# Performance work log

Measured on AMD Instinct MI355X. Metric: run time of the kernel, lower is better.

The kernel has to match this reference:

```python
import jax, jax.numpy as jnp
import numpy as np

THRESH = 0.5
POOL_K = 8  # feature_hw // proto_grid = 128 // 16
EPS = 1e-4
NEG = -1e30


def _avg_pool(x, k):
    # x: [n, c, h, w] -> [n, c, h//k, w//k]
    n, c, h, w = x.shape
    return x.reshape(n, c, h // k, k, w // k, k).mean(axis=(3, 5))


def reference(qry, sup_x, sup_y):
    # squeeze as in forward
    qry = qry[:, 0]          # [B=1, C, H, W]
    sup_x = sup_x[0, :, 0]   # [shot, C, H, W]
    sup_y = sup_y[0]         # [shot, 1, H, W]

    shot, nch, H, W = sup_x.shape

    # grid prototypes via avg pooling
    n_sup = _avg_pool(sup_x, POOL_K)                      # [shot, C, gh, gw]
    y_g = _avg_pool(sup_y, POOL_K)                        # [shot, 1, gh, gw]

    cand = n_sup.reshape(shot, nch, -1).transpose(0, 2, 1).reshape(-1, nch)  # [M, C]
    y_flat = y_g.reshape(-1)                              # [M]

    # threshold mask with fallback chain (thresh -> 0.1 -> all), static shapes
    m1 = y_flat > THRESH
    m2 = y_flat > 0.1
    m_all = jnp.ones_like(m1)
    mask = jnp.where(jnp.any(m1), m1, jnp.where(jnp.any(m2), m2, m_all))  # [M]

    # mean-center and safe L2-normalize prototypes (per proto over channels)
    protos = cand - cand.mean(axis=-1, keepdims=True)
    pro_n = protos / jnp.maximum(jnp.linalg.norm(protos, axis=1, keepdims=True), EPS)  # [M, C]

    # mean-center and safe L2-normalize query (per pixel over channels)
    qc = qry - qry.mean(axis=1, keepdims=True)
    qry_n = qc / jnp.maximum(jnp.linalg.norm(qc, axis=1, keepdims=True), EPS)          # [B, C, H, W]

    # cosine-sim 1x1 conv = GEMM, scaled
    dists = jnp.einsum('bchw,mc->bmhw', qry_n, pro_n) * 20.0                           # [B, M, H, W]

    # masked softmax over prototypes (equivalent to selecting masked subset)
    logits = jnp.where(mask[None, :, None, None], dists, NEG)
    prob = jax.nn.softmax(logits, axis=1)                                              # [B, M, H, W]

    # weighted back-projection and final similarity map
    ch_proto = jnp.einsum('mc,bmhw->bchw', pro_n, prob)                                # [B, C, H, W]
    pred_grid = jnp.sum(qry_n * ch_proto * 20.0, axis=1, keepdims=True)                # [B, 1, H, W]
    return pred_grid


def setup_inputs() -> dict:
    key = jax.random.key(0)
    k1, k2, k3 = jax.random.split(key, 3)
    qry = jax.random.normal(k1, (1, 1, 256, 128, 128), dtype=jnp.float32)
    sup_x = jax.random.normal(k2, (1, 5, 1, 256, 128, 128), dtype=jnp.float32)
    sup_y = jax.random.uniform(k3, (1, 5, 1, 128, 128), dtype=jnp.float32)
    return {"qry": qry, "sup_x": sup_x, "sup_y": sup_y}
```

## Files before the change

kernel.cpp:

```cpp
#include <hip/hip_runtime.h>
#include <math.h>

typedef _Float16 f16x8 __attribute__((ext_vector_type(8)));
typedef float f32x4 __attribute__((ext_vector_type(4)));


__global__ __launch_bounds__(256) void pool_kernel(const float* __restrict__ sup_x,
                                                   const float* __restrict__ sup_y,
                                                   _Float16* __restrict__ pro_raw,
                                                   float* __restrict__ psum,
                                                   float* __restrict__ yv_ws) {
    const int b = blockIdx.x, t = threadIdx.x;
    if (b < 640) {
        __shared__ float hs[8192];
        __shared__ float xa[16][33];
        const int s = b >> 7, rem = b & 127;
        const int gy = rem >> 3, cq = rem & 7;
        const float* base = sup_x + ((size_t)(s * 256 + cq * 32) * 128 + gy * 8) * 128;
#pragma unroll 8
        for (int i = 0; i < 32; ++i) {
            const int run = i * 8 + (t >> 5);
            const float4 v = *(const float4*)(base + ((size_t)(run >> 3) * 128 + (run & 7)) * 128 + (t & 31) * 4);
            hs[i * 256 + t] = v.x + v.y + v.z + v.w;
        }
        __syncthreads();
#pragma unroll
        for (int e0 = 0; e0 < 2; ++e0) {
            const int e = e0 * 256 + t;
            const int c = e >> 4, gx = e & 15;
            float sum = 0.f;
#pragma unroll
            for (int r = 0; r < 8; ++r)
                sum += hs[(c * 8 + r) * 32 + gx * 2] + hs[(c * 8 + r) * 32 + gx * 2 + 1];
            xa[gx][c] = sum * (1.f / 64.f);
        }
        __syncthreads();
        const int mbase = s * 256 + gy * 16;
        if (t < 64) {
            const int gx = t >> 2, gi = t & 3;
            const int m = mbase + gx;
            const int g = cq * 4 + gi;
            f16x8 hv;
#pragma unroll
            for (int j = 0; j < 8; ++j) hv[j] = (_Float16)xa[gx][gi * 8 + j];
            *(f16x8*)(pro_raw + (size_t)m * 256 + ((g ^ (m & 7)) << 3)) = hv;
        } else if (t < 80) {
            const int gx = t - 64;
            float s1 = 0.f, s2 = 0.f;
#pragma unroll
            for (int c = 0; c < 32; ++c) { const float x = xa[gx][c]; s1 += x; s2 += x * x; }
            const int m = mbase + gx;
            psum[m * 16 + cq * 2]     = s1;
            psum[m * 16 + cq * 2 + 1] = s2;
        }
    } else {
        const int r = b - 640;
        const int gy = t >> 4, gx = t & 15;
        const float* base = sup_y + r * 16384 + gy * 1024 + gx * 8;
        float sum = 0.f;
#pragma unroll
        for (int rr = 0; rr < 8; ++rr) {
            const float4 a = *(const float4*)(base + rr * 128);
            const float4 bb = *(const float4*)(base + rr * 128 + 4);
            sum += a.x + a.y + a.z + a.w + bb.x + bb.y + bb.z + bb.w;
        }
        yv_ws[r * 256 + t] = sum * (1.f / 64.f);
    }
}

__device__ __forceinline__ void gload_lds16h(const _Float16* g, _Float16* l) {
    __builtin_amdgcn_global_load_lds((const __attribute__((address_space(1))) unsigned int*)g,
                                     (__attribute__((address_space(3))) unsigned int*)l,
                                     16, 0, 0);
}
__device__ __forceinline__ void gload_lds16f(const float* g, float* l) {
    __builtin_amdgcn_global_load_lds((const __attribute__((address_space(1))) unsigned int*)g,
                                     (__attribute__((address_space(3))) unsigned int*)l,
                                     16, 0, 0);
}

__device__ __forceinline__ void stage_tile(const _Float16* __restrict__ pro_raw,
                                           int tile, _Float16* dst, int w, int l) {
#pragma unroll
    for (int i = 0; i < 8; ++i) {
        const int off = w * 4096 + i * 512 + l * 8;
        gload_lds16h(pro_raw + (size_t)tile * 32768 + off, dst + off);
    }
}

__device__ __forceinline__ void compute_tile(const _Float16* __restrict__ pb,
                                             const float* __restrict__ msp,
                                             const float* __restrict__ asp,
                                             const f16x8 (&bfr)[4][8],
                                             int row, int ln7, int lq,
                                             float (&Sa)[4], float (&Wa)[4]) {
    f32x4 acc[4];
#pragma unroll
    for (int p = 0; p < 4; ++p) acc[p] = (f32x4){0.f, 0.f, 0.f, 0.f};
#pragma unroll
    for (int ks = 0; ks < 8; ++ks) {
        const int ch = (ks * 4 + lq) ^ ln7;
        const f16x8 a = *(const f16x8*)(pb + row * 256 + ch * 8);
#pragma unroll
        for (int p = 0; p < 4; ++p)
            acc[p] = __builtin_amdgcn_mfma_f32_16x16x32_f16(a, bfr[p][ks], acc[p], 0, 0, 0);
    }
    const f32x4 mkv = *(const f32x4*)(msp + lq * 4);
    const f32x4 av  = *(const f32x4*)(asp + lq * 4);
#pragma unroll
    for (int p = 0; p < 4; ++p) {
        float ssum = 0.f, wsum = 0.f;
#pragma unroll
        for (int r = 0; r < 4; ++r) {
            const float d = av[r] * acc[p][r];
            const float e = mkv[r] * __expf(d - 20.f);
            ssum += e; wsum += e * d;
        }
        Sa[p] += ssum; Wa[p] += wsum;
    }
}

__global__ __launch_bounds__(512, 2) void main_kernel(const float* __restrict__ qry,
                                                      const _Float16* __restrict__ pro_raw,
                                                      const float* __restrict__ psum,
                                                      const float* __restrict__ yv_ws,
                                                      float* __restrict__ out) {
    __shared__ __align__(16) _Float16 arena[65536];
    __shared__ float ms[1280];
    __shared__ float alf[1280];
    __shared__ float scr[1024];
    __shared__ float2 stats[64];
    __shared__ int iflags[2];

    float*     qtf  = (float*)arena;
    _Float16*  qs   = arena + 32768;
    _Float16*  buf0 = arena;
    _Float16*  buf1 = arena + 32768;
    float*     red  = (float*)arena;

    const int t = threadIdx.x;
    const int w = t >> 6, l = t & 63;
    const int ln = l & 15, lq = l >> 4;
    const int ln7 = ln & 7;
    const int px0 = blockIdx.x * 64;

    if (t < 2) iflags[t] = 0;
    __syncthreads();

#pragma unroll
    for (int i = 0; i < 8; ++i) {
        const int c = i * 32 + (t >> 4);
        gload_lds16f(qry + (size_t)c * 16384 + px0 + (t & 15) * 4,
                     qtf + i * 2048 + t * 4);
    }

    float yv3[3];
    int f0 = 0, f1 = 0;
#pragma unroll
    for (int k = 0; k < 3; ++k) {
        const int m = t + k * 512;
        if (m < 1280) {
            const f32x4 p0 = *(const f32x4*)(psum + m * 16);
            const f32x4 p1 = *(const f32x4*)(psum + m * 16 + 4);
            const f32x4 p2 = *(const f32x4*)(psum + m * 16 + 8);
            const f32x4 p3 = *(const f32x4*)(psum + m * 16 + 12);
            const float S1 = p0[0] + p0[2] + p1[0] + p1[2] + p2[0] + p2[2] + p3[0] + p3[2];
            const float S2 = p0[1] + p0[3] + p1[1] + p1[3] + p2[1] + p2[3] + p3[1] + p3[3];
            alf[m] = 20.f / fmaxf(sqrtf(fmaxf(S2 - S1 * S1 * (1.f / 256.f), 0.f)), 1e-4f);
            const float y = yv_ws[m];
            yv3[k] = y;
            if (y > 0.5f) f0 = 1;
            if (y > 0.1f) f1 = 1;
        }
    }
    if (f0) atomicOr(&iflags[0], 1);
    if (f1) atomicOr(&iflags[1], 1);
    __syncthreads();
    {
        const int mode = iflags[0] ? 0 : (iflags[1] ? 1 : 2);
#pragma unroll
        for (int k = 0; k < 3; ++k) {
            const int m = t + k * 512;
            if (m < 1280)
                ms[m] = (mode == 0) ? (yv3[k] > 0.5f ? 1.f : 0.f)
                      : (mode == 1) ? (yv3[k] > 0.1f ? 1.f : 0.f) : 1.f;
        }
    }

    {
        const int p = t & 63, q = t >> 6;
        float s1 = 0.f, s2 = 0.f;
        for (int cc = 0; cc < 32; ++cc) {
            const float x = qtf[(q * 32 + cc) * 64 + p];
            s1 += x; s2 += x * x;
        }
        scr[q * 64 + p] = s1; scr[512 + q * 64 + p] = s2;
    }
    __syncthreads();
    if (t < 64) {
        float S1 = 0.f, S2 = 0.f;
        for (int q = 0; q < 8; ++q) { S1 += scr[q * 64 + t]; S2 += scr[512 + q * 64 + t]; }
        const float mu = S1 * (1.f / 256.f);
        const float nrm = sqrtf(fmaxf(S2 - 256.f * mu * mu, 0.f));
        stats[t] = make_float2(mu, 1.f / fmaxf(nrm, 1e-4f));
    }
    __syncthreads();
    {
        const int px = t & 63, e = t >> 6;
        const float2 st = stats[px];
#pragma unroll
        for (int u = 0; u < 4; ++u) {
            const int g = e * 4 + u;
            f16x8 hv;
#pragma unroll
            for (int j = 0; j < 8; ++j)
                hv[j] = (_Float16)((qtf[(g * 8 + j) * 64 + px] - st.x) * st.y);
            *(f16x8*)(qs + px * 256 + ((g ^ (px & 7)) << 3)) = hv;
        }
    }
    __syncthreads();

    stage_tile(pro_raw, 0, buf0, w, l);

    f16x8 bfr[4][8];
#pragma unroll
    for (int p = 0; p < 4; ++p) {
        const int px = p * 16 + ln;
        const int sB = px & 7;
#pragma unroll
        for (int ks = 0; ks < 8; ++ks) {
            const int g = ks * 4 + lq;
            bfr[p][ks] = *(const f16x8*)(qs + px * 256 + ((g ^ sB) << 3));
        }
    }
    __syncthreads();

    stage_tile(pro_raw, 1, buf1, w, l);

    const int row = w * 16 + ln;
    float Sa[4] = {0.f, 0.f, 0.f, 0.f}, Wa[4] = {0.f, 0.f, 0.f, 0.f};

#pragma unroll 1
    for (int tile = 0; tile < 10; ++tile) {
        if (tile < 8) asm volatile("s_waitcnt vmcnt(8)" ::: "memory");
        else          asm volatile("s_waitcnt vmcnt(0)" ::: "memory");
        compute_tile((tile & 1) ? buf1 : buf0,
                     ms + tile * 128 + w * 16, alf + tile * 128 + w * 16,
                     bfr, row, ln7, lq, Sa, Wa);
        if (tile < 8) {
            asm volatile("s_waitcnt lgkmcnt(0)" ::: "memory");
            __builtin_amdgcn_sched_barrier(0);
            stage_tile(pro_raw, tile + 2, (tile & 1) ? buf1 : buf0, w, l);
        }
    }

    __syncthreads();
#pragma unroll
    for (int p = 0; p < 4; ++p) {
        const int px = p * 16 + ln;
        const int slot = (w * 4 + lq + px) & 31;
        red[px * 32 + slot] = Sa[p];
        red[2048 + px * 32 + slot] = Wa[p];
    }
    __syncthreads();
    if (t < 64) {
        float S = 0.f, W = 0.f;
        for (int s = 0; s < 32; ++s) {
            const int slot = (s + t) & 31;
            S += red[t * 32 + slot];
            W += red[2048 + t * 32 + slot];
        }
        out[px0 + t] = W / S;
    }
}

extern "C" void kernel_launch(void* const* d_in, const int* in_sizes, int n_in,
                              void* d_out, int out_size, void* d_ws, size_t ws_size,
                              hipStream_t stream) {
    const float* qry   = (const float*)d_in[0];
    const float* sup_x = (const float*)d_in[1];
    const float* sup_y = (const float*)d_in[2];
    float* out = (float*)d_out;

    char* ws = (char*)d_ws;
    _Float16*  pro_raw = (_Float16*)ws;           ws += 1280 * 256 * 2;
    float*     psum    = (float*)ws;              ws += 1280 * 16 * 4;
    float*     yv_ws   = (float*)ws;

    pool_kernel<<<645, 256, 0, stream>>>(sup_x, sup_y, pro_raw, psum, yv_ws);
    main_kernel<<<256, 512, 0, stream>>>(qry, pro_raw, psum, yv_ws, out);
}
```

Measured before the change: 39.43 us.

## Move query normalization into pool kernel and prefetch tiles early in main

Query mean-centering, normalization and fp16 conversion move from the main kernel into 256 extra blocks of the pool kernel, which write a swizzled fp16 query buffer to workspace. The main kernel then loads its B fragments straight from global memory and issues both prototype tile stages before the mask/alpha setup, shortening its prologue. The cost is an extra round trip of the fp16 query (about 8 MB) through global memory, and a pool kernel that now also reads the 16 MB query while using 64 KB of LDS per block, which may lower its occupancy.

```diff
diff --git a/kernel.cpp b/kernel.cpp
--- a/kernel.cpp
+++ b/kernel.cpp
@@ -6,14 +6,18 @@
 
 
 __global__ __launch_bounds__(256) void pool_kernel(const float* __restrict__ sup_x,
+                                                   const float* __restrict__ qry,
                                                    const float* __restrict__ sup_y,
                                                    _Float16* __restrict__ pro_raw,
                                                    float* __restrict__ psum,
+                                                   _Float16* __restrict__ qn_h,
                                                    float* __restrict__ yv_ws) {
+    __shared__ float sarena[16384];
+    __shared__ float scr[512];
     const int b = blockIdx.x, t = threadIdx.x;
     if (b < 640) {
-        __shared__ float hs[8192];
-        __shared__ float xa[16][33];
+        float* hs = sarena;
+        float (*xa)[33] = (float(*)[33])(sarena + 8192);
         const int s = b >> 7, rem = b & 127;
         const int gy = rem >> 3, cq = rem & 7;
         const float* base = sup_x + ((size_t)(s * 256 + cq * 32) * 128 + gy * 8) * 128;
@@ -53,8 +57,53 @@
             psum[m * 16 + cq * 2]     = s1;
             psum[m * 16 + cq * 2 + 1] = s2;
         }
+    } else if (b < 896) {
+        float* qtf = sarena;
+        const int px0 = (b - 640) * 64;
+#pragma unroll
+        for (int i = 0; i < 16; ++i) {
+            const int c = i * 16 + (t >> 4);
+            __builtin_amdgcn_global_load_lds(
+                (const __attribute__((address_space(1))) unsigned int*)(qry + (size_t)c * 16384 + px0 + (t & 15) * 4),
+                (__attribute__((address_space(3))) unsigned int*)(qtf + c * 64 + (t & 15) * 4),
+                16, 0, 0);
+        }
+        __syncthreads();
+        {
+            const int p = t & 63, q = t >> 6;
+            float s1 = 0.f, s2 = 0.f;
+            for (int cc = 0; cc < 64; ++cc) {
+                const float x = qtf[(q * 64 + cc) * 64 + p];
+                s1 += x; s2 += x * x;
+            }
+            scr[q * 64 + p] = s1; scr[256 + q * 64 + p] = s2;
+        }
+        __syncthreads();
+        __shared__ float2 stats[64];
+        if (t < 64) {
+            float S1 = 0.f, S2 = 0.f;
+#pragma unroll
+            for (int q = 0; q < 4; ++q) { S1 += scr[q * 64 + t]; S2 += scr[256 + q * 64 + t]; }
+            const float mu = S1 * (1.f / 256.f);
+            const float nrm = sqrtf(fmaxf(S2 - 256.f * mu * mu, 0.f));
+            stats[t] = make_float2(mu, 1.f / fmaxf(nrm, 1e-4f));
+        }
+        __syncthreads();
+        {
+            const int px = t >> 2, q4 = t & 3;
+            const float2 st = stats[px];
+#pragma unroll
+            for (int u = 0; u < 8; ++u) {
+                const int g = u * 4 + q4;
+                f16x8 hv;
+#pragma unroll
+                for (int j = 0; j < 8; ++j)
+                    hv[j] = (_Float16)((qtf[(g * 8 + j) * 64 + px] - st.x) * st.y);
+                *(f16x8*)(qn_h + (size_t)(px0 + px) * 256 + ((g ^ (px & 7)) << 3)) = hv;
+            }
+        }
     } else {
-        const int r = b - 640;
+        const int r = b - 896;
         const int gy = t >> 4, gx = t & 15;
         const float* base = sup_y + r * 16384 + gy * 1024 + gx * 8;
         float sum = 0.f;
@@ -69,11 +118,6 @@
 }
 
 __device__ __forceinline__ void gload_lds16h(const _Float16* g, _Float16* l) {
-    __builtin_amdgcn_global_load_lds((const __attribute__((address_space(1))) unsigned int*)g,
-                                     (__attribute__((address_space(3))) unsigned int*)l,
-                                     16, 0, 0);
-}
-__device__ __forceinline__ void gload_lds16f(const float* g, float* l) {
     __builtin_amdgcn_global_load_lds((const __attribute__((address_space(1))) unsigned int*)g,
                                      (__attribute__((address_space(3))) unsigned int*)l,
                                      16, 0, 0);
@@ -120,7 +164,7 @@
     }
 }
 
-__global__ __launch_bounds__(512, 2) void main_kernel(const float* __restrict__ qry,
+__global__ __launch_bounds__(512, 2) void main_kernel(const _Float16* __restrict__ qn_h,
                                                       const _Float16* __restrict__ pro_raw,
                                                       const float* __restrict__ psum,
                                                       const float* __restrict__ yv_ws,
@@ -128,12 +172,8 @@
     __shared__ __align__(16) _Float16 arena[65536];
     __shared__ float ms[1280];
     __shared__ float alf[1280];
-    __shared__ float scr[1024];
-    __shared__ float2 stats[64];
     __shared__ int iflags[2];
 
-    float*     qtf  = (float*)arena;
-    _Float16*  qs   = arena + 32768;
     _Float16*  buf0 = arena;
     _Float16*  buf1 = arena + 32768;
     float*     red  = (float*)arena;
@@ -145,27 +185,36 @@
     const int px0 = blockIdx.x * 64;
 
     if (t < 2) iflags[t] = 0;
-    __syncthreads();
-
-#pragma unroll
-    for (int i = 0; i < 8; ++i) {
-        const int c = i * 32 + (t >> 4);
-        gload_lds16f(qry + (size_t)c * 16384 + px0 + (t & 15) * 4,
-                     qtf + i * 2048 + t * 4);
-    }
-
+
+    f16x8 bfr[4][8];
+#pragma unroll
+    for (int p = 0; p < 4; ++p) {
+        const int px = p * 16 + ln;
+        const int sB = px & 7;
+#pragma unroll
+        for (int ks = 0; ks < 8; ++ks) {
+            const int g = ks * 4 + lq;
+            bfr[p][ks] = *(const f16x8*)(qn_h + (size_t)(px0 + px) * 256 + ((g ^ sB) << 3));
+        }
+    }
+
+    stage_tile(pro_raw, 0, buf0, w, l);
+    stage_tile(pro_raw, 1, buf1, w, l);
+
+    __syncthreads();
     float yv3[3];
     int f0 = 0, f1 = 0;
 #pragma unroll
     for (int k = 0; k < 3; ++k) {
         const int m = t + k * 512;
         if (m < 1280) {
-            const f32x4 p0 = *(const f32x4*)(psum + m * 16);
-            const f32x4 p1 = *(const f32x4*)(psum + m * 16 + 4);
-            const f32x4 p2 = *(const f32x4*)(psum + m * 16 + 8);
-            const f32x4 p3 = *(const f32x4*)(psum + m * 16 + 12);
-            const float S1 = p0[0] + p0[2] + p1[0] + p1[2] + p2[0] + p2[2] + p3[0] + p3[2];
-            const float S2 = p0[1] + p0[3] + p1[1] + p1[3] + p2[1] + p2[3] + p3[1] + p3[3];
+            float S1 = 0.f, S2 = 0.f;
+            const f32x4* pp = (const f32x4*)(psum + m * 16);
+#pragma unroll
+            for (int u = 0; u < 4; ++u) {
+                const f32x4 p = pp[u];
+                S1 += p[0] + p[2]; S2 += p[1] + p[3];
+            }
             alf[m] = 20.f / fmaxf(sqrtf(fmaxf(S2 - S1 * S1 * (1.f / 256.f), 0.f)), 1e-4f);
             const float y = yv_ws[m];
             yv3[k] = y;
@@ -186,56 +235,6 @@
                       : (mode == 1) ? (yv3[k] > 0.1f ? 1.f : 0.f) : 1.f;
         }
     }
-
-    {
-        const int p = t & 63, q = t >> 6;
-        float s1 = 0.f, s2 = 0.f;
-        for (int cc = 0; cc < 32; ++cc) {
-            const float x = qtf[(q * 32 + cc) * 64 + p];
-            s1 += x; s2 += x * x;
-        }
-        scr[q * 64 + p] = s1; scr[512 + q * 64 + p] = s2;
-    }
-    __syncthreads();
-    if (t < 64) {
-        float S1 = 0.f, S2 = 0.f;
-        for (int q = 0; q < 8; ++q) { S1 += scr[q * 64 + t]; S2 += scr[512 + q * 64 + t]; }
-        const float mu = S1 * (1.f / 256.f);
-        const float nrm = sqrtf(fmaxf(S2 - 256.f * mu * mu, 0.f));
-        stats[t] = make_float2(mu, 1.f / fmaxf(nrm, 1e-4f));
-    }
-    __syncthreads();
-    {
-        const int px = t & 63, e = t >> 6;
-        const float2 st = stats[px];
-#pragma unroll
-        for (int u = 0; u < 4; ++u) {
-            const int g = e * 4 + u;
-            f16x8 hv;
-#pragma unroll
-            for (int j = 0; j < 8; ++j)
-                hv[j] = (_Float16)((qtf[(g * 8 + j) * 64 + px] - st.x) * st.y);
-            *(f16x8*)(qs + px * 256 + ((g ^ (px & 7)) << 3)) = hv;
-        }
-    }
-    __syncthreads();
-
-    stage_tile(pro_raw, 0, buf0, w, l);
-
-    f16x8 bfr[4][8];
-#pragma unroll
-    for (int p = 0; p < 4; ++p) {
-        const int px = p * 16 + ln;
-        const int sB = px & 7;
-#pragma unroll
-        for (int ks = 0; ks < 8; ++ks) {
-            const int g = ks * 4 + lq;
-            bfr[p][ks] = *(const f16x8*)(qs + px * 256 + ((g ^ sB) << 3));
-        }
-    }
-    __syncthreads();
-
-    stage_tile(pro_raw, 1, buf1, w, l);
 
     const int row = w * 16 + ln;
     float Sa[4] = {0.f, 0.f, 0.f, 0.f}, Wa[4] = {0.f, 0.f, 0.f, 0.f};
@@ -285,8 +284,9 @@
     char* ws = (char*)d_ws;
     _Float16*  pro_raw = (_Float16*)ws;           ws += 1280 * 256 * 2;
     float*     psum    = (float*)ws;              ws += 1280 * 16 * 4;
-    float*     yv_ws   = (float*)ws;
-
-    pool_kernel<<<645, 256, 0, stream>>>(sup_x, sup_y, pro_raw, psum, yv_ws);
-    main_kernel<<<256, 512, 0, stream>>>(qry, pro_raw, psum, yv_ws, out);
-}
+    float*     yv_ws   = (float*)ws;              ws += 1280 * 4;
+    _Float16*  qn_h    = (_Float16*)ws;
+
+    pool_kernel<<<901, 256, 0, stream>>>(sup_x, qry, sup_y, pro_raw, psum, qn_h, yv_ws);
+    main_kernel<<<256, 512, 0, stream>>>(qn_h, pro_raw, psum, yv_ws, out);
+}
```

Result: slower. 41.50 us (+5.2%).
